# Optimization experiments

Measured on AMD Instinct MI355X. Metric: run time of the kernel, lower is better.

## Reference

```python
import jax, jax.numpy as jnp
import numpy as np

N_TOKENS = 8192
D_MODEL = 1024
D_FF = 4096
N_EXPERTS = 8


def setup_inputs() -> dict:
    key = jax.random.key(0)
    ks = jax.random.split(key, 5)
    scale_in = 1.0 / np.sqrt(D_MODEL)
    x = jax.random.normal(ks[0], (N_TOKENS, D_MODEL), dtype=jnp.float32)
    gate_w = jax.random.normal(ks[1], (D_MODEL, N_EXPERTS), dtype=jnp.float32) * scale_in
    gate_b = jnp.zeros((N_EXPERTS,), dtype=jnp.float32)
    expert_w = jax.random.normal(ks[2], (N_EXPERTS, D_MODEL, D_FF), dtype=jnp.float32) * scale_in
    expert_b = jnp.zeros((N_EXPERTS, D_FF), dtype=jnp.float32)
    return {"x": x, "gate_w": gate_w, "gate_b": gate_b, "expert_w": expert_w, "expert_b": expert_b}


def reference(x, gate_w, gate_b, expert_w, expert_b):
    # Gate: [N, E] logits -> softmax -> top-1 expert per token
    gate_logits = x @ gate_w + gate_b
    gate_probs = jax.nn.softmax(gate_logits, axis=-1)
    top1 = jnp.argmax(gate_probs, axis=-1)  # [N], == argsort(...)[:, -1]

    # Dense all-expert compute, as in the original: [E, N, d_ff]
    expert_outputs = jnp.einsum('nd,edf->enf', x, expert_w) + expert_b[:, None, :]

    # Gather each token's top-1 expert output: [N, d_ff]
    selected = expert_outputs[top1, jnp.arange(x.shape[0])]
    return selected
```

## Files before the change

### kernel.cpp

```cpp
#include <hip/hip_runtime.h>


#define N_TOKENS 8192
#define D_MODEL  1024
#define D_FF     4096
#define N_EXPERTS 8

#define BM 128
#define BN 128
#define BK 32
#define NKT (D_MODEL / BK)
#define MT_MAX (N_TOKENS / BM + N_EXPERTS)
#define NTILES (D_FF / BN)

typedef float  floatx4 __attribute__((ext_vector_type(4)));
typedef short  short8  __attribute__((ext_vector_type(8)));

__device__ __forceinline__ unsigned short f2bf(float f) {
    union { float f; unsigned u; } a; a.f = f;
    return (unsigned short)((a.u + 0x7fffu + ((a.u >> 16) & 1u)) >> 16);
}

#define GLDS(gp, lp) __builtin_amdgcn_global_load_lds( \
    (const __attribute__((address_space(1))) unsigned int*)(const void*)(gp), \
    (__attribute__((address_space(3))) unsigned int*)(void*)(lp), 16, 0, 0)

__global__ void init_counts(int* counts) {
    if (threadIdx.x < N_EXPERTS) counts[threadIdx.x] = 0;
}

__global__ __launch_bounds__(256) void gate_kernel(
    const float* __restrict__ x, const float* __restrict__ gw,
    const float* __restrict__ gb, unsigned short* __restrict__ xb,
    int* __restrict__ top1, int* __restrict__ counts)
{
    int wave = threadIdx.x >> 6;
    int l    = threadIdx.x & 63;
    int n = blockIdx.x * 4 + wave;
    const float4* xr = (const float4*)(x + (size_t)n * D_MODEL);
    float acc[N_EXPERTS];
#pragma unroll
    for (int e = 0; e < N_EXPERTS; ++e) acc[e] = 0.f;

#pragma unroll
    for (int j = 0; j < 4; ++j) {
        int d4 = j * 64 + l;
        float4 v = xr[d4];
        float vv[4] = { v.x, v.y, v.z, v.w };
#pragma unroll
        for (int t = 0; t < 4; ++t) {
            const float4* g = (const float4*)(gw + (size_t)(d4 * 4 + t) * N_EXPERTS);
            float4 g0 = g[0], g1 = g[1];
            acc[0] += vv[t] * g0.x; acc[1] += vv[t] * g0.y;
            acc[2] += vv[t] * g0.z; acc[3] += vv[t] * g0.w;
            acc[4] += vv[t] * g1.x; acc[5] += vv[t] * g1.y;
            acc[6] += vv[t] * g1.z; acc[7] += vv[t] * g1.w;
        }
        union { unsigned short us[4]; uint2 u; } pk;
        pk.us[0] = f2bf(v.x); pk.us[1] = f2bf(v.y);
        pk.us[2] = f2bf(v.z); pk.us[3] = f2bf(v.w);
        ((uint2*)(xb + (size_t)n * D_MODEL))[d4] = pk.u;
    }
#pragma unroll
    for (int e = 0; e < N_EXPERTS; ++e)
        for (int off = 32; off > 0; off >>= 1)
            acc[e] += __shfl_down(acc[e], off);
    if (l == 0) {
        float best = acc[0] + gb[0]; int be = 0;
#pragma unroll
        for (int e = 1; e < N_EXPERTS; ++e) {
            float v = acc[e] + gb[e];
            if (v > best) { best = v; be = e; }
        }
        top1[n] = be;
        atomicAdd(&counts[be], 1);
    }
}

#define WST 68
__global__ __launch_bounds__(256) void wconv_kernel(
    const float* __restrict__ w, unsigned short* __restrict__ wt)
{
    __shared__ unsigned short tt[64 * WST];
    int e  = blockIdx.z;
    int f0 = blockIdx.x * 64;
    int d0 = blockIdx.y * 64;
    int t  = threadIdx.x;
    const float* we = w + (size_t)e * D_MODEL * D_FF + (size_t)d0 * D_FF + f0;

    int fg = (t & 15) * 4;
    int dg = (t >> 4) * 4;
    unsigned short v[4][4];
#pragma unroll
    for (int j = 0; j < 4; ++j) {
        float4 r = *(const float4*)(we + (size_t)(dg + j) * D_FF + fg);
        v[0][j] = f2bf(r.x); v[1][j] = f2bf(r.y);
        v[2][j] = f2bf(r.z); v[3][j] = f2bf(r.w);
    }
#pragma unroll
    for (int i = 0; i < 4; ++i) {
        union { unsigned short us[4]; uint2 u; } pk;
        pk.us[0] = v[i][0]; pk.us[1] = v[i][1];
        pk.us[2] = v[i][2]; pk.us[3] = v[i][3];
        *(uint2*)&tt[(fg + i) * WST + dg] = pk.u;
    }
    __syncthreads();

    unsigned short* wte = wt + (size_t)e * D_FF * D_MODEL + (size_t)f0 * D_MODEL + d0;
    int fr = t >> 3;
    int dr = (t & 7) * 8;
#pragma unroll
    for (int p = 0; p < 2; ++p) {
        int f = fr + p * 32;
        uint2 a = *(const uint2*)&tt[f * WST + dr];
        uint2 b = *(const uint2*)&tt[f * WST + dr + 4];
        uint4 o; o.x = a.x; o.y = a.y; o.z = b.x; o.w = b.y;
        *(uint4*)(wte + (size_t)f * D_MODEL + dr) = o;
    }
}

__global__ void scan_kernel(const int* __restrict__ counts, int* __restrict__ poff,
                            int* __restrict__ tile_expert, int* __restrict__ list,
                            int* __restrict__ cursor)
{
    if (threadIdx.x == 0) {
        int off = 0;
        for (int e = 0; e < N_EXPERTS; ++e) {
            poff[e] = off;
            int nt = (counts[e] + BM - 1) / BM;
            for (int t = 0; t < nt; ++t) tile_expert[off / BM + t] = e;
            off += nt * BM;
        }
        for (int t = off / BM; t < MT_MAX; ++t) tile_expert[t] = -1;
    }
    if (threadIdx.x < N_EXPERTS) cursor[threadIdx.x] = 0;
    for (int i = threadIdx.x; i < MT_MAX * BM; i += blockDim.x) list[i] = -1;
}

__global__ __launch_bounds__(256) void scatter_kernel(
    const int* __restrict__ top1, const int* __restrict__ poff,
    int* __restrict__ cursor, int* __restrict__ list)
{
    int n = blockIdx.x * 256 + threadIdx.x;
    int l = threadIdx.x & 63;
    int e = top1[n];
    int slot = 0;
#pragma unroll
    for (int e0 = 0; e0 < N_EXPERTS; ++e0) {
        unsigned long long m = __ballot(e == e0);
        if (e == e0) {
            int leader = __ffsll((unsigned long long)m) - 1;
            int base = 0;
            if (l == leader) base = atomicAdd(&cursor[e0], __popcll(m));
            base = __shfl(base, leader);
            slot = base + __popcll(m & ((1ull << l) - 1ull));
        }
    }
    list[poff[e] + slot] = n;
}

__global__ __launch_bounds__(256) void gemm_kernel(
    const unsigned short* __restrict__ xb,
    const unsigned short* __restrict__ wt,
    const float* __restrict__ eb,
    const int* __restrict__ tile_expert,
    const int* __restrict__ list,
    float* __restrict__ out)
{
    int bid = blockIdx.x;
    int xcd = bid & 7, w = bid >> 3;
    int mt  = w >> 2;
    int nt  = (xcd << 2) | (w & 3);
    int e = tile_expert[mt];
    if (e < 0) return;
    int n0 = nt * BN;

    __shared__ unsigned short As[2][BM * BK];
    __shared__ unsigned short Bs[2][BN * BK];
    __shared__ int toks[BM];

    int tid = threadIdx.x;
    int lane = tid & 63, wave = tid >> 6;
    if (tid < BM) toks[tid] = list[mt * BM + tid];
    __syncthreads();

    int c0 = (wave * 2 + 0) * 64 + lane;
    int c1 = (wave * 2 + 1) * 64 + lane;
    int ar0 = c0 >> 2, ac0 = (c0 & 3) * 8;
    int ar1 = c1 >> 2, ac1 = (c1 & 3) * 8;
    int ta0 = toks[ar0]; if (ta0 < 0) ta0 = 0;
    int ta1 = toks[ar1]; if (ta1 < 0) ta1 = 0;
    const unsigned short* gA0 = xb + (size_t)ta0 * D_MODEL + ac0;
    const unsigned short* gA1 = xb + (size_t)ta1 * D_MODEL + ac1;
    const unsigned short* wbase = wt + (size_t)e * D_FF * D_MODEL;
    const unsigned short* gB0 = wbase + (size_t)(n0 + ar0) * D_MODEL + ac0;
    const unsigned short* gB1 = wbase + (size_t)(n0 + ar1) * D_MODEL + ac1;
    int o0 = (wave * 2 + 0) * 512;
    int o1 = (wave * 2 + 1) * 512;

    floatx4 acc[4][4];
#pragma unroll
    for (int mi = 0; mi < 4; ++mi)
#pragma unroll
        for (int ni = 0; ni < 4; ++ni)
            acc[mi][ni] = (floatx4){0.f, 0.f, 0.f, 0.f};

    int mw = (wave >> 1) * 64;
    int nw = (wave & 1) * 64;
    int q = lane >> 4, r = lane & 15;

    GLDS(gA0, &As[0][o0]);
    GLDS(gA1, &As[0][o1]);
    GLDS(gB0, &Bs[0][o0]);
    GLDS(gB1, &Bs[0][o1]);

    for (int kt = 0; kt < NKT; ++kt) {
        int cur = kt & 1;
        __syncthreads();
        if (kt + 1 < NKT) {
            int k1 = (kt + 1) * BK;
            GLDS(gA0 + k1, &As[cur ^ 1][o0]);
            GLDS(gA1 + k1, &As[cur ^ 1][o1]);
            GLDS(gB0 + k1, &Bs[cur ^ 1][o0]);
            GLDS(gB1 + k1, &Bs[cur ^ 1][o1]);
        }
        short8 af[4], bf[4];
#pragma unroll
        for (int mi = 0; mi < 4; ++mi)
            af[mi] = *(const short8*)&As[cur][(mw + mi * 16 + r) * BK + q * 8];
#pragma unroll
        for (int ni = 0; ni < 4; ++ni)
            bf[ni] = *(const short8*)&Bs[cur][(nw + ni * 16 + r) * BK + q * 8];
#pragma unroll
        for (int mi = 0; mi < 4; ++mi)
#pragma unroll
            for (int ni = 0; ni < 4; ++ni)
                acc[mi][ni] = __builtin_amdgcn_mfma_f32_16x16x32_bf16(
                    af[mi], bf[ni], acc[mi][ni], 0, 0, 0);
    }

#pragma unroll
    for (int ni = 0; ni < 4; ++ni) {
        int f = n0 + nw + ni * 16 + r;
        float bias = eb[(size_t)e * D_FF + f];
#pragma unroll
        for (int mi = 0; mi < 4; ++mi) {
            int mbase = mw + mi * 16 + q * 4;
#pragma unroll
            for (int i = 0; i < 4; ++i) {
                int tok = toks[mbase + i];
                if (tok >= 0) out[(size_t)tok * D_FF + f] = acc[mi][ni][i] + bias;
            }
        }
    }
}

extern "C" void kernel_launch(void* const* d_in, const int* in_sizes, int n_in,
                              void* d_out, int out_size, void* d_ws, size_t ws_size,
                              hipStream_t stream) {
    const float* x  = (const float*)d_in[0];
    const float* gw = (const float*)d_in[1];
    const float* gb = (const float*)d_in[2];
    const float* ew = (const float*)d_in[3];
    const float* eb = (const float*)d_in[4];
    float* out = (float*)d_out;

    char* ws = (char*)d_ws;
    int* top1        = (int*)ws;
    int* counts      = (int*)(ws + 32768);
    int* cursor      = (int*)(ws + 32768 + 64);
    int* poff        = (int*)(ws + 32768 + 128);
    int* tile_expert = (int*)(ws + 32768 + 256);
    int* list        = (int*)(ws + 36864);
    unsigned short* xb = (unsigned short*)(ws + 131072);
    unsigned short* wt = (unsigned short*)(ws + 131072 + (size_t)N_TOKENS * D_MODEL * 2);

    hipLaunchKernelGGL(init_counts, dim3(1), dim3(64), 0, stream, counts);
    hipLaunchKernelGGL(gate_kernel, dim3(N_TOKENS / 4), dim3(256), 0, stream,
                       x, gw, gb, xb, top1, counts);
    hipLaunchKernelGGL(wconv_kernel, dim3(D_FF / 64, D_MODEL / 64, N_EXPERTS), dim3(256),
                       0, stream, ew, wt);
    hipLaunchKernelGGL(scan_kernel, dim3(1), dim3(256), 0, stream,
                       counts, poff, tile_expert, list, cursor);
    hipLaunchKernelGGL(scatter_kernel, dim3(N_TOKENS / 256), dim3(256), 0, stream,
                       top1, poff, cursor, list);
    hipLaunchKernelGGL(gemm_kernel, dim3(MT_MAX * NTILES), dim3(256), 0, stream,
                       xb, wt, eb, tile_expert, list, out);
}
```

Baseline: 504.4 us.

## Merge prep kernels, single-block routing, and single-buffered BK=64 swizzled GEMM tiles

```diff
diff --git a/kernel.cpp b/kernel.cpp
--- a/kernel.cpp
+++ b/kernel.cpp
@@ -8,10 +8,12 @@
 
 #define BM 128
 #define BN 128
-#define BK 32
+#define BK 64
 #define NKT (D_MODEL / BK)
 #define MT_MAX (N_TOKENS / BM + N_EXPERTS)
 #define NTILES (D_FF / BN)
+#define GATE_BLOCKS (N_TOKENS / 4)
+#define WCONV_BLOCKS ((D_FF / 64) * (D_MODEL / 64) * N_EXPERTS)
 
 typedef float  floatx4 __attribute__((ext_vector_type(4)));
 typedef short  short8  __attribute__((ext_vector_type(8)));
@@ -25,138 +27,149 @@
     (const __attribute__((address_space(1))) unsigned int*)(const void*)(gp), \
     (__attribute__((address_space(3))) unsigned int*)(void*)(lp), 16, 0, 0)
 
-__global__ void init_counts(int* counts) {
-    if (threadIdx.x < N_EXPERTS) counts[threadIdx.x] = 0;
-}
-
-__global__ __launch_bounds__(256) void gate_kernel(
+#define WST 68
+__global__ __launch_bounds__(256) void prep_kernel(
     const float* __restrict__ x, const float* __restrict__ gw,
-    const float* __restrict__ gb, unsigned short* __restrict__ xb,
-    int* __restrict__ top1, int* __restrict__ counts)
+    const float* __restrict__ gb, const float* __restrict__ ew,
+    unsigned short* __restrict__ xb, unsigned short* __restrict__ wt,
+    int* __restrict__ top1)
 {
-    int wave = threadIdx.x >> 6;
-    int l    = threadIdx.x & 63;
-    int n = blockIdx.x * 4 + wave;
-    const float4* xr = (const float4*)(x + (size_t)n * D_MODEL);
-    float acc[N_EXPERTS];
-#pragma unroll
-    for (int e = 0; e < N_EXPERTS; ++e) acc[e] = 0.f;
-
-#pragma unroll
-    for (int j = 0; j < 4; ++j) {
-        int d4 = j * 64 + l;
-        float4 v = xr[d4];
-        float vv[4] = { v.x, v.y, v.z, v.w };
-#pragma unroll
-        for (int t = 0; t < 4; ++t) {
-            const float4* g = (const float4*)(gw + (size_t)(d4 * 4 + t) * N_EXPERTS);
-            float4 g0 = g[0], g1 = g[1];
-            acc[0] += vv[t] * g0.x; acc[1] += vv[t] * g0.y;
-            acc[2] += vv[t] * g0.z; acc[3] += vv[t] * g0.w;
-            acc[4] += vv[t] * g1.x; acc[5] += vv[t] * g1.y;
-            acc[6] += vv[t] * g1.z; acc[7] += vv[t] * g1.w;
-        }
-        union { unsigned short us[4]; uint2 u; } pk;
-        pk.us[0] = f2bf(v.x); pk.us[1] = f2bf(v.y);
-        pk.us[2] = f2bf(v.z); pk.us[3] = f2bf(v.w);
-        ((uint2*)(xb + (size_t)n * D_MODEL))[d4] = pk.u;
-    }
-#pragma unroll
-    for (int e = 0; e < N_EXPERTS; ++e)
-        for (int off = 32; off > 0; off >>= 1)
-            acc[e] += __shfl_down(acc[e], off);
-    if (l == 0) {
-        float best = acc[0] + gb[0]; int be = 0;
-#pragma unroll
-        for (int e = 1; e < N_EXPERTS; ++e) {
-            float v = acc[e] + gb[e];
-            if (v > best) { best = v; be = e; }
-        }
-        top1[n] = be;
-        atomicAdd(&counts[be], 1);
-    }
-}
-
-#define WST 68
-__global__ __launch_bounds__(256) void wconv_kernel(
-    const float* __restrict__ w, unsigned short* __restrict__ wt)
+    if (blockIdx.x < GATE_BLOCKS) {
+        int wave = threadIdx.x >> 6;
+        int l    = threadIdx.x & 63;
+        int n = blockIdx.x * 4 + wave;
+        const float4* xr = (const float4*)(x + (size_t)n * D_MODEL);
+        float acc[N_EXPERTS];
+#pragma unroll
+        for (int e = 0; e < N_EXPERTS; ++e) acc[e] = 0.f;
+#pragma unroll
+        for (int j = 0; j < 4; ++j) {
+            int d4 = j * 64 + l;
+            float4 v = xr[d4];
+            float vv[4] = { v.x, v.y, v.z, v.w };
+#pragma unroll
+            for (int t = 0; t < 4; ++t) {
+                const float4* g = (const float4*)(gw + (size_t)(d4 * 4 + t) * N_EXPERTS);
+                float4 g0 = g[0], g1 = g[1];
+                acc[0] += vv[t] * g0.x; acc[1] += vv[t] * g0.y;
+                acc[2] += vv[t] * g0.z; acc[3] += vv[t] * g0.w;
+                acc[4] += vv[t] * g1.x; acc[5] += vv[t] * g1.y;
+                acc[6] += vv[t] * g1.z; acc[7] += vv[t] * g1.w;
+            }
+            union { unsigned short us[4]; uint2 u; } pk;
+            pk.us[0] = f2bf(v.x); pk.us[1] = f2bf(v.y);
+            pk.us[2] = f2bf(v.z); pk.us[3] = f2bf(v.w);
+            ((uint2*)(xb + (size_t)n * D_MODEL))[d4] = pk.u;
+        }
+#pragma unroll
+        for (int e = 0; e < N_EXPERTS; ++e)
+            for (int off = 32; off > 0; off >>= 1)
+                acc[e] += __shfl_down(acc[e], off);
+        if (l == 0) {
+            float best = acc[0] + gb[0]; int be = 0;
+#pragma unroll
+            for (int e = 1; e < N_EXPERTS; ++e) {
+                float v = acc[e] + gb[e];
+                if (v > best) { best = v; be = e; }
+            }
+            top1[n] = be;
+        }
+    } else {
+        __shared__ unsigned short tt[64 * WST];
+        int b  = blockIdx.x - GATE_BLOCKS;
+        int f0 = (b & 63) * 64;
+        int d0 = ((b >> 6) & 15) * 64;
+        int e  = b >> 10;
+        int t  = threadIdx.x;
+        const float* we = ew + (size_t)e * D_MODEL * D_FF + (size_t)d0 * D_FF + f0;
+        int fg = (t & 15) * 4;
+        int dg = (t >> 4) * 4;
+        unsigned short v[4][4];
+#pragma unroll
+        for (int j = 0; j < 4; ++j) {
+            float4 r = *(const float4*)(we + (size_t)(dg + j) * D_FF + fg);
+            v[0][j] = f2bf(r.x); v[1][j] = f2bf(r.y);
+            v[2][j] = f2bf(r.z); v[3][j] = f2bf(r.w);
+        }
+#pragma unroll
+        for (int i = 0; i < 4; ++i) {
+            union { unsigned short us[4]; uint2 u; } pk;
+            pk.us[0] = v[i][0]; pk.us[1] = v[i][1];
+            pk.us[2] = v[i][2]; pk.us[3] = v[i][3];
+            *(uint2*)&tt[(fg + i) * WST + dg] = pk.u;
+        }
+        __syncthreads();
+        unsigned short* wte = wt + (size_t)e * D_FF * D_MODEL + (size_t)f0 * D_MODEL + d0;
+        int fr = t >> 3;
+        int dr = (t & 7) * 8;
+#pragma unroll
+        for (int p = 0; p < 2; ++p) {
+            int f = fr + p * 32;
+            uint2 a = *(const uint2*)&tt[f * WST + dr];
+            uint2 c = *(const uint2*)&tt[f * WST + dr + 4];
+            uint4 o; o.x = a.x; o.y = a.y; o.z = c.x; o.w = c.y;
+            *(uint4*)(wte + (size_t)f * D_MODEL + dr) = o;
+        }
+    }
+}
+
+__global__ __launch_bounds__(1024) void route_kernel(
+    const int* __restrict__ top1, int* __restrict__ tile_expert, int* __restrict__ list)
 {
-    __shared__ unsigned short tt[64 * WST];
-    int e  = blockIdx.z;
-    int f0 = blockIdx.x * 64;
-    int d0 = blockIdx.y * 64;
-    int t  = threadIdx.x;
-    const float* we = w + (size_t)e * D_MODEL * D_FF + (size_t)d0 * D_FF + f0;
-
-    int fg = (t & 15) * 4;
-    int dg = (t >> 4) * 4;
-    unsigned short v[4][4];
-#pragma unroll
-    for (int j = 0; j < 4; ++j) {
-        float4 r = *(const float4*)(we + (size_t)(dg + j) * D_FF + fg);
-        v[0][j] = f2bf(r.x); v[1][j] = f2bf(r.y);
-        v[2][j] = f2bf(r.z); v[3][j] = f2bf(r.w);
-    }
-#pragma unroll
-    for (int i = 0; i < 4; ++i) {
-        union { unsigned short us[4]; uint2 u; } pk;
-        pk.us[0] = v[i][0]; pk.us[1] = v[i][1];
-        pk.us[2] = v[i][2]; pk.us[3] = v[i][3];
-        *(uint2*)&tt[(fg + i) * WST + dg] = pk.u;
-    }
+    __shared__ int wtot[16][N_EXPERTS];
+    __shared__ int wbase[16][N_EXPERTS];
+    __shared__ int pofs[N_EXPERTS];
+    int t = threadIdx.x, wv = t >> 6, l = t & 63;
+
+    for (int i = t; i < MT_MAX * BM; i += 1024) list[i] = -1;
+
+    int e8[8];
+    const int4* tp = (const int4*)(top1 + t * 8);
+    int4 a = tp[0], b = tp[1];
+    e8[0] = a.x; e8[1] = a.y; e8[2] = a.z; e8[3] = a.w;
+    e8[4] = b.x; e8[5] = b.y; e8[6] = b.z; e8[7] = b.w;
+    int c[N_EXPERTS], s[N_EXPERTS];
+#pragma unroll
+    for (int e = 0; e < N_EXPERTS; ++e) c[e] = 0;
+#pragma unroll
+    for (int j = 0; j < 8; ++j) c[e8[j]]++;
+#pragma unroll
+    for (int e = 0; e < N_EXPERTS; ++e) s[e] = c[e];
+    for (int off = 1; off < 64; off <<= 1) {
+#pragma unroll
+        for (int e = 0; e < N_EXPERTS; ++e) {
+            int v = __shfl_up(s[e], off);
+            if (l >= off) s[e] += v;
+        }
+    }
+    if (l == 63)
+#pragma unroll
+        for (int e = 0; e < N_EXPERTS; ++e) wtot[wv][e] = s[e];
     __syncthreads();
-
-    unsigned short* wte = wt + (size_t)e * D_FF * D_MODEL + (size_t)f0 * D_MODEL + d0;
-    int fr = t >> 3;
-    int dr = (t & 7) * 8;
-#pragma unroll
-    for (int p = 0; p < 2; ++p) {
-        int f = fr + p * 32;
-        uint2 a = *(const uint2*)&tt[f * WST + dr];
-        uint2 b = *(const uint2*)&tt[f * WST + dr + 4];
-        uint4 o; o.x = a.x; o.y = a.y; o.z = b.x; o.w = b.y;
-        *(uint4*)(wte + (size_t)f * D_MODEL + dr) = o;
-    }
-}
-
-__global__ void scan_kernel(const int* __restrict__ counts, int* __restrict__ poff,
-                            int* __restrict__ tile_expert, int* __restrict__ list,
-                            int* __restrict__ cursor)
-{
-    if (threadIdx.x == 0) {
+    if (t == 0) {
+        int cnt[N_EXPERTS];
+        for (int e = 0; e < N_EXPERTS; ++e) {
+            cnt[e] = 0;
+            for (int w = 0; w < 16; ++w) { wbase[w][e] = cnt[e]; cnt[e] += wtot[w][e]; }
+        }
         int off = 0;
         for (int e = 0; e < N_EXPERTS; ++e) {
-            poff[e] = off;
-            int nt = (counts[e] + BM - 1) / BM;
-            for (int t = 0; t < nt; ++t) tile_expert[off / BM + t] = e;
-            off += nt * BM;
-        }
-        for (int t = off / BM; t < MT_MAX; ++t) tile_expert[t] = -1;
-    }
-    if (threadIdx.x < N_EXPERTS) cursor[threadIdx.x] = 0;
-    for (int i = threadIdx.x; i < MT_MAX * BM; i += blockDim.x) list[i] = -1;
-}
-
-__global__ __launch_bounds__(256) void scatter_kernel(
-    const int* __restrict__ top1, const int* __restrict__ poff,
-    int* __restrict__ cursor, int* __restrict__ list)
-{
-    int n = blockIdx.x * 256 + threadIdx.x;
-    int l = threadIdx.x & 63;
-    int e = top1[n];
-    int slot = 0;
-#pragma unroll
-    for (int e0 = 0; e0 < N_EXPERTS; ++e0) {
-        unsigned long long m = __ballot(e == e0);
-        if (e == e0) {
-            int leader = __ffsll((unsigned long long)m) - 1;
-            int base = 0;
-            if (l == leader) base = atomicAdd(&cursor[e0], __popcll(m));
-            base = __shfl(base, leader);
-            slot = base + __popcll(m & ((1ull << l) - 1ull));
-        }
-    }
-    list[poff[e] + slot] = n;
+            pofs[e] = off;
+            int ntl = (cnt[e] + BM - 1) / BM;
+            for (int k = 0; k < ntl; ++k) tile_expert[off / BM + k] = e;
+            off += ntl * BM;
+        }
+        for (int k = off / BM; k < MT_MAX; ++k) tile_expert[k] = -1;
+    }
+    __syncthreads();
+    int base[N_EXPERTS];
+#pragma unroll
+    for (int e = 0; e < N_EXPERTS; ++e) base[e] = pofs[e] + wbase[wv][e] + s[e] - c[e];
+#pragma unroll
+    for (int j = 0; j < 8; ++j) {
+        int e = e8[j];
+        list[base[e]++] = t * 8 + j;
+    }
 }
 
 __global__ __launch_bounds__(256) void gemm_kernel(
@@ -175,8 +188,8 @@
     if (e < 0) return;
     int n0 = nt * BN;
 
-    __shared__ unsigned short As[2][BM * BK];
-    __shared__ unsigned short Bs[2][BN * BK];
+    __shared__ unsigned short As[BM * BK];
+    __shared__ unsigned short Bs[BN * BK];
     __shared__ int toks[BM];
 
     int tid = threadIdx.x;
@@ -184,19 +197,17 @@
     if (tid < BM) toks[tid] = list[mt * BM + tid];
     __syncthreads();
 
-    int c0 = (wave * 2 + 0) * 64 + lane;
-    int c1 = (wave * 2 + 1) * 64 + lane;
-    int ar0 = c0 >> 2, ac0 = (c0 & 3) * 8;
-    int ar1 = c1 >> 2, ac1 = (c1 & 3) * 8;
-    int ta0 = toks[ar0]; if (ta0 < 0) ta0 = 0;
-    int ta1 = toks[ar1]; if (ta1 < 0) ta1 = 0;
-    const unsigned short* gA0 = xb + (size_t)ta0 * D_MODEL + ac0;
-    const unsigned short* gA1 = xb + (size_t)ta1 * D_MODEL + ac1;
+    const unsigned short* gA[4];
+    const unsigned short* gB[4];
     const unsigned short* wbase = wt + (size_t)e * D_FF * D_MODEL;
-    const unsigned short* gB0 = wbase + (size_t)(n0 + ar0) * D_MODEL + ac0;
-    const unsigned short* gB1 = wbase + (size_t)(n0 + ar1) * D_MODEL + ac1;
-    int o0 = (wave * 2 + 0) * 512;
-    int o1 = (wave * 2 + 1) * 512;
+#pragma unroll
+    for (int i = 0; i < 4; ++i) {
+        int s = wave * 256 + i * 64 + lane;
+        int row = s >> 3, c8 = (s & 7) ^ (row & 7);
+        int ta = toks[row]; if (ta < 0) ta = 0;
+        gA[i] = xb + (size_t)ta * D_MODEL + c8 * 8;
+        gB[i] = wbase + (size_t)(n0 + row) * D_MODEL + c8 * 8;
+    }
 
     floatx4 acc[4][4];
 #pragma unroll
@@ -208,35 +219,36 @@
     int mw = (wave >> 1) * 64;
     int nw = (wave & 1) * 64;
     int q = lane >> 4, r = lane & 15;
-
-    GLDS(gA0, &As[0][o0]);
-    GLDS(gA1, &As[0][o1]);
-    GLDS(gB0, &Bs[0][o0]);
-    GLDS(gB1, &Bs[0][o1]);
+    int xr = r & 7;
+    int ra[4], rb[4];
+#pragma unroll
+    for (int i = 0; i < 4; ++i) { ra[i] = (mw + i * 16 + r) * 8; rb[i] = (nw + i * 16 + r) * 8; }
 
     for (int kt = 0; kt < NKT; ++kt) {
-        int cur = kt & 1;
+        int k0 = kt * BK;
+#pragma unroll
+        for (int i = 0; i < 4; ++i) GLDS(gA[i] + k0, &As[(wave * 256 + i * 64) * 8]);
+#pragma unroll
+        for (int i = 0; i < 4; ++i) GLDS(gB[i] + k0, &Bs[(wave * 256 + i * 64) * 8]);
         __syncthreads();
-        if (kt + 1 < NKT) {
-            int k1 = (kt + 1) * BK;
-            GLDS(gA0 + k1, &As[cur ^ 1][o0]);
-            GLDS(gA1 + k1, &As[cur ^ 1][o1]);
-            GLDS(gB0 + k1, &Bs[cur ^ 1][o0]);
-            GLDS(gB1 + k1, &Bs[cur ^ 1][o1]);
-        }
-        short8 af[4], bf[4];
-#pragma unroll
-        for (int mi = 0; mi < 4; ++mi)
-            af[mi] = *(const short8*)&As[cur][(mw + mi * 16 + r) * BK + q * 8];
-#pragma unroll
-        for (int ni = 0; ni < 4; ++ni)
-            bf[ni] = *(const short8*)&Bs[cur][(nw + ni * 16 + r) * BK + q * 8];
-#pragma unroll
-        for (int mi = 0; mi < 4; ++mi)
+#pragma unroll
+        for (int ks = 0; ks < 2; ++ks) {
+            int cq = (ks * 4 + q) ^ xr;
+            short8 af[4], bf[4];
+#pragma unroll
+            for (int mi = 0; mi < 4; ++mi)
+                af[mi] = *(const short8*)&As[(ra[mi] + cq) * 8];
 #pragma unroll
             for (int ni = 0; ni < 4; ++ni)
-                acc[mi][ni] = __builtin_amdgcn_mfma_f32_16x16x32_bf16(
-                    af[mi], bf[ni], acc[mi][ni], 0, 0, 0);
+                bf[ni] = *(const short8*)&Bs[(rb[ni] + cq) * 8];
+#pragma unroll
+            for (int mi = 0; mi < 4; ++mi)
+#pragma unroll
+                for (int ni = 0; ni < 4; ++ni)
+                    acc[mi][ni] = __builtin_amdgcn_mfma_f32_16x16x32_bf16(
+                        af[mi], bf[ni], acc[mi][ni], 0, 0, 0);
+        }
+        __syncthreads();
     }
 
 #pragma unroll
@@ -267,23 +279,15 @@
 
     char* ws = (char*)d_ws;
     int* top1        = (int*)ws;
-    int* counts      = (int*)(ws + 32768);
-    int* cursor      = (int*)(ws + 32768 + 64);
-    int* poff        = (int*)(ws + 32768 + 128);
-    int* tile_expert = (int*)(ws + 32768 + 256);
+    int* tile_expert = (int*)(ws + 32768);
     int* list        = (int*)(ws + 36864);
     unsigned short* xb = (unsigned short*)(ws + 131072);
     unsigned short* wt = (unsigned short*)(ws + 131072 + (size_t)N_TOKENS * D_MODEL * 2);
 
-    hipLaunchKernelGGL(init_counts, dim3(1), dim3(64), 0, stream, counts);
-    hipLaunchKernelGGL(gate_kernel, dim3(N_TOKENS / 4), dim3(256), 0, stream,
-                       x, gw, gb, xb, top1, counts);
-    hipLaunchKernelGGL(wconv_kernel, dim3(D_FF / 64, D_MODEL / 64, N_EXPERTS), dim3(256),
-                       0, stream, ew, wt);
-    hipLaunchKernelGGL(scan_kernel, dim3(1), dim3(256), 0, stream,
-                       counts, poff, tile_expert, list, cursor);
-    hipLaunchKernelGGL(scatter_kernel, dim3(N_TOKENS / 256), dim3(256), 0, stream,
-                       top1, poff, cursor, list);
+    hipLaunchKernelGGL(prep_kernel, dim3(GATE_BLOCKS + WCONV_BLOCKS), dim3(256), 0, stream,
+                       x, gw, gb, ew, xb, wt, top1);
+    hipLaunchKernelGGL(route_kernel, dim3(1), dim3(1024), 0, stream,
+                       top1, tile_expert, list);
     hipLaunchKernelGGL(gemm_kernel, dim3(MT_MAX * NTILES), dim3(256), 0, stream,
                        xb, wt, eb, tile_expert, list, out);
 }
```

New measurement: 439.7 us. -12.8%, faster.
